# Kernel tuning notes

Hardware: AMD Instinct MI355X
Metric: run time of the kernel (lower is better)

The kernel has to match this reference:

```python
import jax, jax.numpy as jnp
import numpy as np

N, E = 20000, 320000          # nodes, edges (avg in-degree ~16)
F_IN, EMB, T, OUT = 40, 40, 5, 2
F_T = EMB // T                # per-tower output width = 8
EPS_STD, EPS_GN = 1e-5, 1e-5


def _lin_init(k, fan_in, fan_out, extra=()):
    return jax.random.normal(k, (*extra, fan_in, fan_out), jnp.float32) / np.sqrt(fan_in)


def setup_inputs() -> dict:
    key = jax.random.key(0)
    ks = jax.random.split(key, 8)
    # deg histogram in init: all 20000 nodes with degree 16 -> avg_deg['log'] = log(16+1)
    return dict(
        x=jax.random.normal(ks[0], (N, F_IN), jnp.float32),
        edge_index=jax.random.randint(ks[1], (2, E), 0, N),
        W_pre=_lin_init(ks[2], 2 * F_IN, F_IN, (T,)),   # per-tower pre-MLP
        b_pre=jnp.zeros((T, F_IN), jnp.float32),
        W_post=_lin_init(ks[3], 13 * F_IN, F_T, (T,)),  # (4 agg * 3 scalers + 1 residual) * F_in
        b_post=jnp.zeros((T, F_T), jnp.float32),
        W_lin=_lin_init(ks[4], T * F_T, EMB),           # PNAConv final mixing linear
        b_lin=jnp.zeros((EMB,), jnp.float32),
        gn_weight=jnp.ones((EMB,), jnp.float32),
        gn_bias=jnp.zeros((EMB,), jnp.float32),
        gn_mean_scale=jnp.ones((EMB,), jnp.float32),
        W1=_lin_init(ks[5], EMB, EMB),                  # head hidden linear
        b1=jnp.zeros((EMB,), jnp.float32),
        W2=_lin_init(ks[6], EMB, OUT),                  # head output linear
        b2=jnp.zeros((OUT,), jnp.float32),
        avg_deg_log=jnp.float32(np.log(17.0)),
    )


def _pna_conv(x, src, dst, W_pre, b_pre, W_post, b_post, W_lin, b_lin, avg_deg_log):
    xi, xj = x[dst], x[src]                              # gather: [E, F]
    h = jnp.concatenate([xi, xj], axis=-1)               # [E, 2F]
    m = jnp.einsum('ef,tfg->etg', h, W_pre) + b_pre      # per-tower messages [E, T, F]
    cnt = jax.ops.segment_sum(jnp.ones((E,), m.dtype), dst, num_segments=N)  # in-degree [N]
    denom = jnp.maximum(cnt, 1.0)[:, None, None]
    mean = jax.ops.segment_sum(m, dst, num_segments=N) / denom
    mean2 = jax.ops.segment_sum(m * m, dst, num_segments=N) / denom
    std = jnp.sqrt(jax.nn.relu(mean2 - mean * mean) + EPS_STD)
    has = (cnt > 0)[:, None, None]
    mn = jnp.where(has, jax.ops.segment_min(m, dst, num_segments=N), 0.0)
    mx = jnp.where(has, jax.ops.segment_max(m, dst, num_segments=N), 0.0)
    agg = jnp.concatenate([mean, mn, mx, std], axis=-1)  # [N, T, 4F]
    deg = jnp.maximum(cnt, 1.0)[:, None, None]
    logd = jnp.log(deg + 1.0)
    out = jnp.concatenate(
        [agg, agg * (logd / avg_deg_log), agg * (avg_deg_log / logd)], axis=-1)  # [N, T, 12F]
    out = jnp.concatenate(
        [jnp.broadcast_to(x[:, None, :], (N, T, x.shape[-1])), out], axis=-1)    # [N, T, 13F]
    out = jnp.einsum('ntf,tfg->ntg', out, W_post) + b_post                       # [N, T, F_T]
    return out.reshape(N, T * F_T) @ W_lin + b_lin


def _graph_norm(x, w, b, mean_scale):
    mean = jnp.mean(x, axis=0, keepdims=True)
    out = x - mean_scale * mean
    var = jnp.mean(out * out, axis=0, keepdims=True)
    return w * out / jnp.sqrt(var + EPS_GN) + b


def reference(x, edge_index, W_pre, b_pre, W_post, b_post, W_lin, b_lin,
              gn_weight, gn_bias, gn_mean_scale, W1, b1, W2, b2, avg_deg_log):
    src, dst = edge_index[0], edge_index[1]
    h = _pna_conv(x, src, dst, W_pre, b_pre, W_post, b_post, W_lin, b_lin, avg_deg_log)
    h = jax.nn.relu(_graph_norm(h, gn_weight, gn_bias, gn_mean_scale))
    h = jax.nn.relu(h @ W1 + b1)   # dropout_rate=None -> no dropout
    return h @ W2 + b2
```

## Files before the change

kernel.cpp:

```cpp
#include <hip/hip_runtime.h>
#include <math.h>

#define N_NODES 20000
#define N_EDGES 320000
#define F_IN 40
#define T_TOW 5
#define EMB 40
#define NPB_PRE 16
#define NBLK_MIX 313
#define NPB_PM 16
#define NBLK_PM 1250
#define PLANE (T_TOW * N_NODES * 40)
#define ECHUNK 16
#define STRIDE 64

typedef __attribute__((ext_vector_type(8))) _Float16 half8;
typedef __attribute__((ext_vector_type(2))) _Float16 half2_t;

#define WS_STATS   0
#define WS_CURSOR  320
#define WS_SSRC    80384
#define WS_MS      5200384
#define WS_MD      13200384
#define WS_AGG     21200384
#define WS_XPOST   53200384
#define WS_H0T     69200384
#define WS_PART    72400384

__global__ __launch_bounds__(256) void k_pre(const float* __restrict__ x,
                                             const float* __restrict__ W_pre,
                                             const float* __restrict__ b_pre,
                                             const float* __restrict__ W_post,
                                             const float* __restrict__ b_post,
                                             _Float16* __restrict__ mS,
                                             _Float16* __restrict__ mD,
                                             float* __restrict__ xpostT,
                                             int* __restrict__ cursor) {
  const int tid = threadIdx.x;
  const int n0 = blockIdx.x * NPB_PRE;
  if (tid < NPB_PRE) cursor[n0 + tid] = (n0 + tid) * STRIDE;
  const bool statlane = tid < 200;
  const int q = tid - 200;
  const bool xplane = (q >= 0 && q < 40);
  const int tc = statlane ? tid : 199;
  const int t = tc / 40, g = tc - t * 40;
  const int t2 = xplane ? q / 8 : 0, g2 = xplane ? q - (q / 8) * 8 : 0;
  float wA[40], wB[40];
  const float* Wt = W_pre + t * 3200;
#pragma unroll
  for (int j = 0; j < 40; ++j) {
    wA[j] = statlane ? Wt[j * 40 + g] : W_post[t2 * 4160 + j * 8 + g2];
    wB[j] = statlane ? Wt[(40 + j) * 40 + g] : 0.f;
  }
  const float bias = statlane ? b_pre[t * 40 + g] : b_post[t2 * 8 + g2];
  for (int ni = 0; ni < NPB_PRE; ++ni) {
    const int n = n0 + ni;
    const float* xr = x + n * F_IN;
    float aA = bias, aB = 0.f;
#pragma unroll
    for (int j = 0; j < 40; j += 4) {
      const float4 xv = *(const float4*)(xr + j);
      aA += xv.x * wA[j] + xv.y * wA[j + 1] + xv.z * wA[j + 2] + xv.w * wA[j + 3];
      aB += xv.x * wB[j] + xv.y * wB[j + 1] + xv.z * wB[j + 2] + xv.w * wB[j + 3];
    }
    if (statlane) {
      mD[n * 200 + tc] = (_Float16)aA;
      mS[n * 200 + tc] = (_Float16)aB;
    } else if (xplane) {
      xpostT[t2 * (N_NODES * 8) + n * 8 + g2] = aA;
    }
  }
}

__global__ __launch_bounds__(256) void k_scatter(const int* __restrict__ src,
                                                 const int* __restrict__ dst,
                                                 int* __restrict__ cursor,
                                                 int* __restrict__ ssrc) {
  int i = blockIdx.x * 256 + threadIdx.x;
  if (i < N_EDGES) {
    int d = dst[i];
    int pos = atomicAdd(&cursor[d], 1);
    ssrc[pos] = src[i];
  }
}

__global__ __launch_bounds__(256) void k_edge(const _Float16* __restrict__ mS,
                                              const _Float16* __restrict__ mD,
                                              const int* __restrict__ cursor,
                                              const int* __restrict__ ssrc,
                                              _Float16* __restrict__ aggS) {
  const int lane = threadIdx.x & 63;
  const int wv = threadIdx.x >> 6;
  const int n = blockIdx.x * 4 + wv;
  const int r0 = n * STRIDE;
  const int r1 = __builtin_amdgcn_readfirstlane(cursor[n]);
  const int cnt = r1 - r0;
  const int cpa = lane;
  const bool bact = lane < 36;
  const int cpb = bact ? 64 + lane : 99;
  const half2_t mda = ((const half2_t*)(mD + n * 200))[cpa];
  const half2_t mdb = ((const half2_t*)(mD + n * 200))[cpb];

  const _Float16 HINF = (_Float16)65504.f;
  half2_t suma = {0, 0}, ssqa = {0, 0}, sumb = {0, 0}, ssqb = {0, 0};
  half2_t mna = {HINF, HINF}, mxa = {-HINF, -HINF};
  half2_t mnb = {HINF, HINF}, mxb = {-HINF, -HINF};
  half2_t va = {0, 0}, vb = {0, 0};

  if (cnt > 0) {
    for (int p = r0; p < r1; p += ECHUNK) {
      half2_t ha[ECHUNK], hb[ECHUNK];
#pragma unroll
      for (int i = 0; i < ECHUNK; ++i) {
        const int qe = (p + i < r1) ? (p + i) : (r1 - 1);
        const int s = __builtin_amdgcn_readfirstlane(ssrc[qe]);
        const half2_t* row = (const half2_t*)(mS + s * 200);
        ha[i] = row[cpa];
        hb[i] = row[cpb];
      }
#pragma unroll
      for (int i = 0; i < ECHUNK; ++i) {
        suma += ha[i];
        ssqa += ha[i] * ha[i];
        mna = __builtin_elementwise_min(mna, ha[i]);
        mxa = __builtin_elementwise_max(mxa, ha[i]);
        sumb += hb[i];
        ssqb += hb[i] * hb[i];
        mnb = __builtin_elementwise_min(mnb, hb[i]);
        mxb = __builtin_elementwise_max(mxb, hb[i]);
      }
      va = ha[ECHUNK - 1];
      vb = hb[ECHUNK - 1];
    }
  }

  const int padded = ((cnt + ECHUNK - 1) / ECHUNK) * ECHUNK;
  const float d = (float)(padded - cnt);
  const float inv = (cnt > 0) ? 1.f / (float)cnt : 0.f;
#pragma unroll
  for (int set = 0; set < 2; ++set) {
    if (set == 1 && !bact) break;
    const int cp = set == 0 ? cpa : cpb;
    const half2_t sum2 = set == 0 ? suma : sumb;
    const half2_t ssq2 = set == 0 ? ssqa : ssqb;
    const half2_t mn2 = set == 0 ? mna : mnb;
    const half2_t mx2 = set == 0 ? mxa : mxb;
    const half2_t vl2 = set == 0 ? va : vb;
    const half2_t md2 = set == 0 ? mda : mdb;
    half2_t omean, omn, omx, osd;
#pragma unroll
    for (int j = 0; j < 2; ++j) {
      float mean, mnf, mxf, sd;
      if (cnt > 0) {
        const float vl = (float)vl2[j];
        const float sf = (float)sum2[j] - d * vl;
        const float qf = (float)ssq2[j] - d * vl * vl;
        const float msm = sf * inv;
        const float var = qf * inv - msm * msm;
        sd = sqrtf(fmaxf(var, 0.f) + 1e-5f);
        const float mdf = (float)md2[j];
        mean = mdf + msm;
        mnf = mdf + (float)mn2[j];
        mxf = mdf + (float)mx2[j];
      } else {
        mean = 0.f; mnf = 0.f; mxf = 0.f; sd = sqrtf(1e-5f);
      }
      omean[j] = (_Float16)mean;
      omn[j] = (_Float16)mnf;
      omx[j] = (_Float16)mxf;
      osd[j] = (_Float16)sd;
    }
    const int t = cp / 20, g = 2 * (cp - t * 20);
    half2_t* a = (half2_t*)(aggS + (t * N_NODES + n) * 40 + g);
    a[0] = omean;
    *(half2_t*)((_Float16*)a + PLANE) = omn;
    *(half2_t*)((_Float16*)a + 2 * PLANE) = omx;
    *(half2_t*)((_Float16*)a + 3 * PLANE) = osd;
  }
}

__global__ __launch_bounds__(320) void k_postmix(const _Float16* __restrict__ aggS,
                                                 const int* __restrict__ cursor,
                                                 const float* __restrict__ W_post,
                                                 const float* __restrict__ avg_dl,
                                                 const float* __restrict__ xpostT,
                                                 const float* __restrict__ W_lin,
                                                 const float* __restrict__ b_lin,
                                                 float* __restrict__ h0T,
                                                 float* __restrict__ partial) {
  __shared__ float sP[16 * 41];
  const int tid = threadIdx.x;
  const int t = tid >> 6;
  const int l = tid & 63;
  const int s = l >> 4;
  const int ni = l & 15;
  const int n0 = blockIdx.x * NPB_PM;
  const int n = n0 + ni;

  const int cnt = cursor[n] - n * STRIDE;
  const float degf = fmaxf((float)cnt, 1.f);
  const float logd = logf(degf + 1.f);
  const float avg = avg_dl[0];
  const float s1v = logd / avg, s2v = avg / logd;

  half8 cur[5];
  {
    const half8* ar = (const half8*)(aggS + s * PLANE + ((size_t)t * N_NODES + n) * 40);
#pragma unroll
    for (int q2 = 0; q2 < 5; ++q2) cur[q2] = ar[q2];
  }
  const float* Wt = W_post + t * 4160 + (40 + s * 40) * 8;
  float A[8], B[8], C[8];
#pragma unroll
  for (int g = 0; g < 8; ++g) { A[g] = 0.f; B[g] = 0.f; C[g] = 0.f; }
#pragma unroll
  for (int f = 0; f < 40; ++f) {
    const float val = (float)cur[f >> 3][f & 7];
    const float* wrow = Wt + f * 8;
#pragma unroll
    for (int g = 0; g < 8; ++g) {
      A[g] = fmaf(val, wrow[g], A[g]);
      B[g] = fmaf(val, wrow[1280 + g], B[g]);
      C[g] = fmaf(val, wrow[2560 + g], C[g]);
    }
  }
  float v[8];
#pragma unroll
  for (int g = 0; g < 8; ++g) {
    v[g] = A[g] + s1v * B[g] + s2v * C[g];
    v[g] += __shfl_xor(v[g], 16, 64);
    v[g] += __shfl_xor(v[g], 32, 64);
  }
  if (s == 0) {
    const float* xp = xpostT + t * (N_NODES * 8) + n * 8;
#pragma unroll
    for (int g = 0; g < 8; ++g) sP[ni * 41 + t * 8 + g] = v[g] + xp[g];
  }
  __syncthreads();

  const int cq = l & 3;
  const int nb = l >> 2;
  const int nB = n0 + nb;
  const int cc = t * 8 + cq * 2;
  float a0 = b_lin[cc], a1 = b_lin[cc + 1];
  for (int k = 0; k < 40; ++k) {
    const float p = sP[nb * 41 + k];
    const float2 w = *(const float2*)(W_lin + k * EMB + cc);
    a0 = fmaf(p, w.x, a0);
    a1 = fmaf(p, w.y, a1);
  }
  h0T[cc * N_NODES + nB] = a0;
  h0T[(cc + 1) * N_NODES + nB] = a1;
  float q0 = a0 * a0, q1 = a1 * a1;
#pragma unroll
  for (int m = 4; m <= 32; m <<= 1) {
    a0 += __shfl_xor(a0, m, 64);
    a1 += __shfl_xor(a1, m, 64);
    q0 += __shfl_xor(q0, m, 64);
    q1 += __shfl_xor(q1, m, 64);
  }
  if (nb == 0) {
    float* pb = partial + blockIdx.x * 80;
    pb[cc] = a0;
    pb[cc + 1] = a1;
    pb[40 + cc] = q0;
    pb[40 + cc + 1] = q1;
  }
}

__global__ __launch_bounds__(256) void k_stats(const float* __restrict__ partial,
                                               float* __restrict__ S1,
                                               float* __restrict__ S2) {
  const int col = blockIdx.x;
  const int tid = threadIdx.x;
  __shared__ float red[4];
  float s = 0.f;
  for (int b = tid; b < NBLK_PM; b += 256) s += partial[b * 80 + col];
#pragma unroll
  for (int m = 32; m >= 1; m >>= 1) s += __shfl_xor(s, m, 64);
  if ((tid & 63) == 0) red[tid >> 6] = s;
  __syncthreads();
  if (tid == 0) {
    const float tot = (red[0] + red[1]) + (red[2] + red[3]);
    if (col < 40) S1[col] = tot;
    else S2[col - 40] = tot;
  }
}

__global__ __launch_bounds__(256) void k_head(const float* __restrict__ S1,
                                              const float* __restrict__ S2,
                                              const float* __restrict__ h0T,
                                              const float* __restrict__ gn_w,
                                              const float* __restrict__ gn_b,
                                              const float* __restrict__ gn_ms,
                                              const float* __restrict__ W1,
                                              const float* __restrict__ b1,
                                              const float* __restrict__ W2,
                                              const float* __restrict__ b2,
                                              float* __restrict__ out) {
  __shared__ float sV[64 * 41];
  __shared__ float sH[64 * 41];
  const int tid = threadIdx.x;
  const int n0 = blockIdx.x * 64;
  const float invN = 1.f / (float)N_NODES;
  for (int i = 0; i < 10; ++i) {
    const int idx = tid + i * 256;
    const int e = idx >> 6, r = idx & 63;
    const int nn0 = n0 + r;
    const int nn = (nn0 < N_NODES) ? nn0 : 0;
    const float M = S1[e] * invN;
    const float ms = gn_ms[e];
    const float var = S2[e] * invN - ms * (2.f - ms) * M * M;
    const float sc = gn_w[e] / sqrtf(var + 1e-5f);
    const float he = h0T[e * N_NODES + nn];
    sV[r * 41 + e] = fmaxf((he - ms * M) * sc + gn_b[e], 0.f);
  }
  __syncthreads();
  const int wv = tid >> 6, lane = tid & 63;
  const int c0 = wv * 10;
  float acc[10];
#pragma unroll
  for (int j = 0; j < 10; ++j) acc[j] = b1[c0 + j];
  for (int k = 0; k < 40; ++k) {
    const float p = sV[lane * 41 + k];
    const float* w = W1 + k * EMB + c0;
#pragma unroll
    for (int j = 0; j < 10; ++j) acc[j] = fmaf(p, w[j], acc[j]);
  }
#pragma unroll
  for (int j = 0; j < 10; ++j) sH[lane * 41 + c0 + j] = fmaxf(acc[j], 0.f);
  __syncthreads();
  if (tid < 64) {
    const int n = n0 + tid;
    if (n < N_NODES) {
      float o0 = b2[0], o1 = b2[1];
      const float* hr = sH + tid * 41;
#pragma unroll
      for (int k = 0; k < 40; ++k) {
        const float r = hr[k];
        o0 = fmaf(r, W2[k * 2], o0);
        o1 = fmaf(r, W2[k * 2 + 1], o1);
      }
      out[n * 2] = o0;
      out[n * 2 + 1] = o1;
    }
  }
}

extern "C" void kernel_launch(void* const* d_in, const int* in_sizes, int n_in,
                              void* d_out, int out_size, void* d_ws, size_t ws_size,
                              hipStream_t stream) {
  const float* x      = (const float*)d_in[0];
  const int*   ei     = (const int*)d_in[1];
  const float* W_pre  = (const float*)d_in[2];
  const float* b_pre  = (const float*)d_in[3];
  const float* W_post = (const float*)d_in[4];
  const float* b_post = (const float*)d_in[5];
  const float* W_lin  = (const float*)d_in[6];
  const float* b_lin  = (const float*)d_in[7];
  const float* gn_w   = (const float*)d_in[8];
  const float* gn_b   = (const float*)d_in[9];
  const float* gn_ms  = (const float*)d_in[10];
  const float* W1     = (const float*)d_in[11];
  const float* b1     = (const float*)d_in[12];
  const float* W2     = (const float*)d_in[13];
  const float* b2     = (const float*)d_in[14];
  const float* avg_dl = (const float*)d_in[15];
  float* out = (float*)d_out;

  char* ws = (char*)d_ws;
  float* S1   = (float*)(ws + WS_STATS);
  float* S2   = S1 + 40;
  int* cursor = (int*)(ws + WS_CURSOR);
  int* ssrc   = (int*)(ws + WS_SSRC);
  _Float16* mS   = (_Float16*)(ws + WS_MS);
  _Float16* mD   = (_Float16*)(ws + WS_MD);
  _Float16* aggS = (_Float16*)(ws + WS_AGG);
  float* xpostT  = (float*)(ws + WS_XPOST);
  float* h0T     = (float*)(ws + WS_H0T);
  float* part    = (float*)(ws + WS_PART);
  const int* e_src = ei;
  const int* e_dst = ei + N_EDGES;

  k_pre<<<N_NODES / NPB_PRE, 256, 0, stream>>>(x, W_pre, b_pre, W_post, b_post,
                                               mS, mD, xpostT, cursor);
  k_scatter<<<(N_EDGES + 255) / 256, 256, 0, stream>>>(e_src, e_dst, cursor, ssrc);
  k_edge<<<N_NODES / 4, 256, 0, stream>>>(mS, mD, cursor, ssrc, aggS);
  k_postmix<<<NBLK_PM, 320, 0, stream>>>(aggS, cursor, W_post, avg_dl,
                                         xpostT, W_lin, b_lin, h0T, part);
  k_stats<<<80, 256, 0, stream>>>(part, S1, S2);
  k_head<<<NBLK_MIX, 256, 0, stream>>>(S1, S2, h0T, gn_w, gn_b, gn_ms,
                                       W1, b1, W2, b2, out);
}
```

Measured before the change: 237.5 us.

## Use MFMA for post-aggregation GEMM with node-interleaved agg layout

Changes the aggregate buffer from four separate planes to a per-(tower,node) interleaved 160-element row. The post-MLP scaler GEMM now runs on 16x16x32 fp16 MFMA instructions with W_post fragments preloaded in registers, and each block covers 64 nodes in 4 tiles instead of 16. This is meant to replace scalar FMA loops and cut block count, at the cost of fp16 rounding of weights and clamped tail handling for the last partial block.

New measurement: 191.7 us. -19.3%, faster.

```diff
diff --git a/kernel.cpp b/kernel.cpp
--- a/kernel.cpp
+++ b/kernel.cpp
@@ -8,14 +8,13 @@
 #define EMB 40
 #define NPB_PRE 16
 #define NBLK_MIX 313
-#define NPB_PM 16
-#define NBLK_PM 1250
-#define PLANE (T_TOW * N_NODES * 40)
+#define NBLK_PM 313
 #define ECHUNK 16
 #define STRIDE 64
 
 typedef __attribute__((ext_vector_type(8))) _Float16 half8;
 typedef __attribute__((ext_vector_type(2))) _Float16 half2_t;
+typedef __attribute__((ext_vector_type(4))) float f32x4;
 
 #define WS_STATS   0
 #define WS_CURSOR  320
@@ -171,15 +170,15 @@
       osd[j] = (_Float16)sd;
     }
     const int t = cp / 20, g = 2 * (cp - t * 20);
-    half2_t* a = (half2_t*)(aggS + (t * N_NODES + n) * 40 + g);
-    a[0] = omean;
-    *(half2_t*)((_Float16*)a + PLANE) = omn;
-    *(half2_t*)((_Float16*)a + 2 * PLANE) = omx;
-    *(half2_t*)((_Float16*)a + 3 * PLANE) = osd;
-  }
-}
-
-__global__ __launch_bounds__(320) void k_postmix(const _Float16* __restrict__ aggS,
+    _Float16* abase = aggS + ((size_t)t * N_NODES + n) * 160 + g;
+    *(half2_t*)(abase) = omean;
+    *(half2_t*)(abase + 40) = omn;
+    *(half2_t*)(abase + 80) = omx;
+    *(half2_t*)(abase + 120) = osd;
+  }
+}
+
+__global__ __launch_bounds__(320) void k_postmix(const _Float16* __restrict__ aggT,
                                                  const int* __restrict__ cursor,
                                                  const float* __restrict__ W_post,
                                                  const float* __restrict__ avg_dl,
@@ -188,83 +187,91 @@
                                                  const float* __restrict__ b_lin,
                                                  float* __restrict__ h0T,
                                                  float* __restrict__ partial) {
-  __shared__ float sP[16 * 41];
+  __shared__ float sP[64 * 41];
   const int tid = threadIdx.x;
   const int t = tid >> 6;
   const int l = tid & 63;
-  const int s = l >> 4;
-  const int ni = l & 15;
-  const int n0 = blockIdx.x * NPB_PM;
-  const int n = n0 + ni;
-
-  const int cnt = cursor[n] - n * STRIDE;
-  const float degf = fmaxf((float)cnt, 1.f);
-  const float logd = logf(degf + 1.f);
+  const int n0 = blockIdx.x * 64;
+  const int c = l & 15;
+  const int kg = l >> 4;
+
+  const float* Wt = W_post + t * 4160;
+  half8 b1f[5], b2f[5];
+#pragma unroll
+  for (int ks = 0; ks < 5; ++ks) {
+#pragma unroll
+    for (int j = 0; j < 8; ++j) {
+      const int k = ks * 32 + kg * 8 + j;
+      const float w1v = (c < 8) ? Wt[(40 + k) * 8 + c] : Wt[(200 + k) * 8 + (c - 8)];
+      const float w2v = (c < 8) ? Wt[(360 + k) * 8 + c] : 0.f;
+      b1f[ks][j] = (_Float16)w1v;
+      b2f[ks][j] = (_Float16)w2v;
+    }
+  }
   const float avg = avg_dl[0];
-  const float s1v = logd / avg, s2v = avg / logd;
-
-  half8 cur[5];
-  {
-    const half8* ar = (const half8*)(aggS + s * PLANE + ((size_t)t * N_NODES + n) * 40);
-#pragma unroll
-    for (int q2 = 0; q2 < 5; ++q2) cur[q2] = ar[q2];
-  }
-  const float* Wt = W_post + t * 4160 + (40 + s * 40) * 8;
-  float A[8], B[8], C[8];
-#pragma unroll
-  for (int g = 0; g < 8; ++g) { A[g] = 0.f; B[g] = 0.f; C[g] = 0.f; }
-#pragma unroll
-  for (int f = 0; f < 40; ++f) {
-    const float val = (float)cur[f >> 3][f & 7];
-    const float* wrow = Wt + f * 8;
-#pragma unroll
-    for (int g = 0; g < 8; ++g) {
-      A[g] = fmaf(val, wrow[g], A[g]);
-      B[g] = fmaf(val, wrow[1280 + g], B[g]);
-      C[g] = fmaf(val, wrow[2560 + g], C[g]);
-    }
-  }
-  float v[8];
-#pragma unroll
-  for (int g = 0; g < 8; ++g) {
-    v[g] = A[g] + s1v * B[g] + s2v * C[g];
-    v[g] += __shfl_xor(v[g], 16, 64);
-    v[g] += __shfl_xor(v[g], 32, 64);
-  }
-  if (s == 0) {
-    const float* xp = xpostT + t * (N_NODES * 8) + n * 8;
-#pragma unroll
-    for (int g = 0; g < 8; ++g) sP[ni * 41 + t * 8 + g] = v[g] + xp[g];
+
+  for (int tile = 0; tile < 4; ++tile) {
+    const int nb = n0 + tile * 16;
+    int nA = nb + c;
+    if (nA >= N_NODES) nA = N_NODES - 1;
+    const half8* ar = (const half8*)(aggT + ((size_t)t * N_NODES + nA) * 160);
+    half8 af[5];
+#pragma unroll
+    for (int ks = 0; ks < 5; ++ks) af[ks] = ar[ks * 4 + kg];
+    f32x4 acc1 = {0.f, 0.f, 0.f, 0.f}, acc2 = {0.f, 0.f, 0.f, 0.f};
+#pragma unroll
+    for (int ks = 0; ks < 5; ++ks) {
+      acc1 = __builtin_amdgcn_mfma_f32_16x16x32_f16(af[ks], b1f[ks], acc1, 0, 0, 0);
+      acc2 = __builtin_amdgcn_mfma_f32_16x16x32_f16(af[ks], b2f[ks], acc2, 0, 0, 0);
+    }
+    float bp[4];
+#pragma unroll
+    for (int r = 0; r < 4; ++r) bp[r] = __shfl_xor(acc1[r], 8, 64);
+    if (c < 8) {
+#pragma unroll
+      for (int r = 0; r < 4; ++r) {
+        const int nn0 = nb + kg * 4 + r;
+        const int nn = (nn0 < N_NODES) ? nn0 : N_NODES - 1;
+        const int cnt = cursor[nn] - nn * STRIDE;
+        const float ld = logf(fmaxf((float)cnt, 1.f) + 1.f);
+        const float s1 = ld / avg, s2 = avg / ld;
+        const float xp = xpostT[t * (N_NODES * 8) + nn * 8 + c];
+        sP[(tile * 16 + kg * 4 + r) * 41 + t * 8 + c] =
+            acc1[r] + s1 * bp[r] + s2 * acc2[r] + xp;
+      }
+    }
   }
   __syncthreads();
 
-  const int cq = l & 3;
-  const int nb = l >> 2;
-  const int nB = n0 + nb;
-  const int cc = t * 8 + cq * 2;
-  float a0 = b_lin[cc], a1 = b_lin[cc + 1];
+  const int c0 = t * 8;
+  float acc[8];
+#pragma unroll
+  for (int j = 0; j < 8; ++j) acc[j] = b_lin[c0 + j];
   for (int k = 0; k < 40; ++k) {
-    const float p = sP[nb * 41 + k];
-    const float2 w = *(const float2*)(W_lin + k * EMB + cc);
-    a0 = fmaf(p, w.x, a0);
-    a1 = fmaf(p, w.y, a1);
-  }
-  h0T[cc * N_NODES + nB] = a0;
-  h0T[(cc + 1) * N_NODES + nB] = a1;
-  float q0 = a0 * a0, q1 = a1 * a1;
-#pragma unroll
-  for (int m = 4; m <= 32; m <<= 1) {
-    a0 += __shfl_xor(a0, m, 64);
-    a1 += __shfl_xor(a1, m, 64);
-    q0 += __shfl_xor(q0, m, 64);
-    q1 += __shfl_xor(q1, m, 64);
-  }
-  if (nb == 0) {
-    float* pb = partial + blockIdx.x * 80;
-    pb[cc] = a0;
-    pb[cc + 1] = a1;
-    pb[40 + cc] = q0;
-    pb[40 + cc + 1] = q1;
+    const float p = sP[l * 41 + k];
+    const float* w = W_lin + k * EMB + c0;
+#pragma unroll
+    for (int j = 0; j < 8; ++j) acc[j] = fmaf(p, w[j], acc[j]);
+  }
+  const int n = n0 + l;
+  const bool ok = n < N_NODES;
+  if (ok) {
+#pragma unroll
+    for (int j = 0; j < 8; ++j) h0T[(c0 + j) * N_NODES + n] = acc[j];
+  }
+#pragma unroll
+  for (int j = 0; j < 8; ++j) {
+    float sv = ok ? acc[j] : 0.f;
+    float qv = sv * sv;
+#pragma unroll
+    for (int m = 32; m >= 1; m >>= 1) {
+      sv += __shfl_xor(sv, m, 64);
+      qv += __shfl_xor(qv, m, 64);
+    }
+    if (l == 0) {
+      partial[blockIdx.x * 80 + c0 + j] = sv;
+      partial[blockIdx.x * 80 + 40 + c0 + j] = qv;
+    }
   }
 }
 
```
